# Kernel tuning notes

Hardware: AMD Instinct MI355X
Metric: run time of the kernel (lower is better)

Reference implementation:

```python
import jax, jax.numpy as jnp
import numpy as np

D_MODEL = 1024
NUM_HEADS = 16
D_K = D_MODEL // NUM_HEADS  # 64
THETA = 10000.0
MAX_SEQ_LEN = 2048


def _trunc_normal(key, shape, std):
    # approximate trunc_normal_(mean=0, std, a=-3*std, b=3*std)
    u = jax.random.truncated_normal(key, -3.0, 3.0, shape, dtype=jnp.float32)
    return u * std


def setup_inputs() -> dict:
    key = jax.random.key(0)
    ks = jax.random.split(key, 5)
    x = jax.random.normal(ks[0], (2, 2048, D_MODEL), dtype=jnp.float32)
    token_positions = jnp.arange(2048, dtype=jnp.int64 if jax.config.jax_enable_x64 else jnp.int32)
    sigma = 2.0 / (D_MODEL + D_MODEL)
    Wq = _trunc_normal(ks[1], (D_MODEL, D_MODEL), sigma)
    Wk = _trunc_normal(ks[2], (D_MODEL, D_MODEL), sigma)
    Wv = _trunc_normal(ks[3], (D_MODEL, D_MODEL), sigma)
    Wo = _trunc_normal(ks[4], (D_MODEL, D_MODEL), sigma)
    return {"in_features": x, "Wq": Wq, "Wk": Wk, "Wv": Wv, "Wo": Wo,
            "token_positions": token_positions}


def _rope(x, cos_phi, sin_phi):
    # x: (..., seq, d_k); cos/sin: (seq, d_k//2)
    x_even = x[..., 0::2]
    x_odd = x[..., 1::2]
    y_even = x_even * cos_phi - x_odd * sin_phi
    y_odd = x_even * sin_phi + x_odd * cos_phi
    # interleave back
    y = jnp.stack([y_even, y_odd], axis=-1)
    return y.reshape(x.shape)


def reference(in_features, Wq, Wk, Wv, Wo, token_positions):
    b, s, d = in_features.shape
    h, dk = NUM_HEADS, D_K
    # projections: weight is (d_out, d_in)
    q = jnp.einsum('bsd,ed->bse', in_features, Wq)
    k = jnp.einsum('bsd,ed->bse', in_features, Wk)
    v = jnp.einsum('bsd,ed->bse', in_features, Wv)
    # split heads: (b, h, s, dk)
    q = q.reshape(b, s, h, dk).transpose(0, 2, 1, 3)
    k = k.reshape(b, s, h, dk).transpose(0, 2, 1, 3)
    v = v.reshape(b, s, h, dk).transpose(0, 2, 1, 3)
    # RoPE tables
    inv_freq = 1.0 / (THETA ** (jnp.arange(0, dk, 2, dtype=jnp.float32) / dk))
    phi = token_positions.astype(jnp.float32)[:, None] * inv_freq[None, :]  # (s, dk/2)
    cos_phi, sin_phi = jnp.cos(phi), jnp.sin(phi)
    q = _rope(q, cos_phi, sin_phi)
    k = _rope(k, cos_phi, sin_phi)
    # causal mask
    mask = jnp.tril(jnp.ones((s, s), dtype=bool))
    scores = jnp.einsum('bhqd,bhkd->bhqk', q, k) / jnp.sqrt(jnp.float32(dk))
    scores = jnp.where(mask, scores, -jnp.inf)
    attn = jax.nn.softmax(scores, axis=-1)
    out = jnp.einsum('bhqk,bhkd->bhqd', attn, v)
    out = out.transpose(0, 2, 1, 3).reshape(b, s, d)
    return jnp.einsum('bsd,ed->bse', out, Wo)
```

## Files before the change

kernel.cpp:

```cpp
#include <hip/hip_runtime.h>
#include <hip/hip_bf16.h>
#include <math.h>

#define S_  2048
#define DM_ 1024

typedef unsigned short u16;
typedef __attribute__((ext_vector_type(8))) short short8;
typedef __attribute__((ext_vector_type(4))) float f32x4;

__device__ __forceinline__ u16 f2bf(float f) {
  unsigned u = __float_as_uint(f);
  u += 0x7fffu + ((u >> 16) & 1u);
  return (u16)(u >> 16);
}
__device__ __forceinline__ float bf2f(u16 h) {
  return __uint_as_float((unsigned)h << 16);
}
__device__ __forceinline__ unsigned pack_bf2(float a, float b) {
  union { __hip_bfloat162 h2; unsigned u; } cv;
  cv.h2 = __float22bfloat162_rn(float2{a, b});
  return cv.u;
}
__device__ __forceinline__ void cp16(const void* g, void* l) {
  __builtin_amdgcn_global_load_lds(
      (const __attribute__((address_space(1))) unsigned*)(uintptr_t)g,
      (__attribute__((address_space(3))) unsigned*)(unsigned)(uintptr_t)l, 16, 0, 0);
}

struct CastArgs { const float* src[5]; u16* dst[5]; int n[5]; };

__global__ __launch_bounds__(256) void cast_kernel(CastArgs a) {
  const int z = blockIdx.y;
  const int i = (blockIdx.x * 256 + threadIdx.x) * 8;
  if (i >= a.n[z]) return;
  const float4* s = (const float4*)(a.src[z] + i);
  float4 v0 = s[0], v1 = s[1];
  short8 r;
  r[0] = (short)f2bf(v0.x); r[1] = (short)f2bf(v0.y);
  r[2] = (short)f2bf(v0.z); r[3] = (short)f2bf(v0.w);
  r[4] = (short)f2bf(v1.x); r[5] = (short)f2bf(v1.y);
  r[6] = (short)f2bf(v1.z); r[7] = (short)f2bf(v1.w);
  *(short8*)(a.dst[z] + i) = r;
}

struct GemmArgs { const u16* A; const u16* W[3]; void* out[3]; int modes; };

template<int GXL>
__global__ __launch_bounds__(256, 2) void gemm_mfma(GemmArgs g) {
  constexpr int BM = 128, BN = 64;
  constexpr int ABYTES = BM * 64 * 2;
  constexpr int SLOT = ABYTES + BN * 64 * 2;
  __shared__ __align__(16) char lds[3 * SLOT];

  const int tid = threadIdx.x, lane = tid & 63, w = tid >> 6;
  const int wm = w >> 1, wn = w & 1;
  const int t = lane & 15, u = lane >> 4;
  const int l3 = lane >> 3, l7 = lane & 7;
  const int z = blockIdx.z;

  const int nwg = (int)gridDim.y << GXL;
  const int flat = (int)blockIdx.x + ((int)blockIdx.y << GXL);
  const int swz = (flat & 7) * (nwg >> 3) + (flat >> 3);
  const int m0 = (swz >> GXL) * BM;
  const int n0 = (swz & ((1 << GXL) - 1)) * BN;

  const u16* __restrict__ A = g.A;
  const u16* __restrict__ W = g.W[z];

  const int axor = l7 << 4;
  const int ksw = (l7 ^ l3) * 8;
  const u16* Ab = A + (size_t)(m0 + l3) * 1024 + ksw;
  const u16* Wb = W + (size_t)(n0 + l3) * 1024 + ksw;

  auto stg = [&](char* sb, int kt) {
    #pragma unroll
    for (int r = 0; r < 4; r++)
      cp16(Ab + (size_t)(w * 4 + r) * 8192 + kt * 64, sb + (w * 4 + r) * 1024);
    #pragma unroll
    for (int r = 0; r < 2; r++)
      cp16(Wb + (size_t)(w * 2 + r) * 8192 + kt * 64, sb + ABYTES + (w * 2 + r) * 1024);
  };

  const f32x4 fz = {0.f, 0.f, 0.f, 0.f};
  f32x4 acc[4][2];
  #pragma unroll
  for (int i = 0; i < 4; i++) { acc[i][0] = fz; acc[i][1] = fz; }

  stg(lds, 0);
  stg(lds + SLOT, 1);
  asm volatile("s_waitcnt vmcnt(6)" ::: "memory");
  __builtin_amdgcn_s_barrier();

  int rs_ = 0, ss_ = 2;
  for (int kt = 0; kt < 16; kt++) {
    const char* cs = lds + rs_ * SLOT;
    if (kt + 2 < 16) stg(lds + ss_ * SLOT, kt + 2);

    short8 af[2][4], bfr[2][2];
    #pragma unroll
    for (int ks = 0; ks < 2; ks++) {
      const int co = (ks * 64 + u * 16) ^ axor;
      const char* ap = cs + (wm * 64 + t) * 128 + co;
      const char* bp = cs + ABYTES + (wn * 32 + t) * 128 + co;
      #pragma unroll
      for (int mf = 0; mf < 4; mf++) af[ks][mf] = *(const short8*)(ap + mf * 2048);
      #pragma unroll
      for (int nf = 0; nf < 2; nf++) bfr[ks][nf] = *(const short8*)(bp + nf * 2048);
    }
    asm volatile("s_waitcnt lgkmcnt(0)" ::: "memory");
    __builtin_amdgcn_sched_barrier(0);
    __builtin_amdgcn_s_setprio(1);
    #pragma unroll
    for (int ks = 0; ks < 2; ks++)
      #pragma unroll
      for (int mf = 0; mf < 4; mf++)
        #pragma unroll
        for (int nf = 0; nf < 2; nf++)
          acc[mf][nf] = __builtin_amdgcn_mfma_f32_16x16x32_bf16(af[ks][mf], bfr[ks][nf], acc[mf][nf], 0, 0, 0);
    __builtin_amdgcn_s_setprio(0);

    if (kt + 2 < 16)      { asm volatile("s_waitcnt vmcnt(6)" ::: "memory"); }
    else if (kt + 1 < 16) { asm volatile("s_waitcnt vmcnt(0)" ::: "memory"); }
    __builtin_amdgcn_s_barrier();
    rs_ = (rs_ == 2) ? 0 : rs_ + 1;
    ss_ = (ss_ == 2) ? 0 : ss_ + 1;
  }

  const int mode = (g.modes >> (2 * z)) & 3;
  const int rbase = m0 + wm * 64 + u * 4;
  const int cbase = n0 + wn * 32 + t;
  if (mode == 0) {
    u16* O = (u16*)g.out[z];
    #pragma unroll
    for (int mt = 0; mt < 4; mt++)
      #pragma unroll
      for (int nt = 0; nt < 2; nt++)
        #pragma unroll
        for (int r = 0; r < 4; r++)
          O[(size_t)(rbase + mt * 16 + r) * 1024 + cbase + nt * 16] = f2bf(acc[mt][nt][r]);
  } else if (mode == 1) {
    u16* O = (u16*)g.out[z];
    #pragma unroll
    for (int mt = 0; mt < 4; mt++)
      #pragma unroll
      for (int nt = 0; nt < 2; nt++) {
        int gr = rbase + mt * 16;
        int b = gr >> 11, s0 = gr & (S_ - 1);
        int gc = cbase + nt * 16;
        int h = gc >> 6, d = gc & 63;
        ushort4 v;
        v.x = f2bf(acc[mt][nt][0]); v.y = f2bf(acc[mt][nt][1]);
        v.z = f2bf(acc[mt][nt][2]); v.w = f2bf(acc[mt][nt][3]);
        *(ushort4*)&O[(size_t)((b * 16 + h) * 64 + d) * 2048 + s0] = v;
      }
  } else {
    float* O = (float*)g.out[z];
    #pragma unroll
    for (int mt = 0; mt < 4; mt++)
      #pragma unroll
      for (int nt = 0; nt < 2; nt++)
        #pragma unroll
        for (int r = 0; r < 4; r++)
          O[(size_t)(rbase + mt * 16 + r) * 1024 + cbase + nt * 16] = acc[mt][nt][r];
  }
}

__global__ __launch_bounds__(256) void rope_kernel(u16* qb, u16* kb, const int* __restrict__ tp) {
  const int isq = (blockIdx.y == 0);
  u16* p = isq ? qb : kb;
  const float outscale = isq ? 0.18033688011112042f : 1.0f;
  const int i = (blockIdx.x * 256 + threadIdx.x) * 8;
  const int s = (i >> 10) & (S_ - 1);
  const int d = i & 63;
  const float pos = (float)tp[s];
  short8 v = *(short8*)(p + i);
  #pragma unroll
  for (int j = 0; j < 4; j++) {
    float inv = exp2f(-(float)(d + 2 * j) * 0.20762050593046439f);
    float phi = pos * inv;
    float sn, cs;
    sincosf(phi, &sn, &cs);
    float xe = bf2f((u16)v[2 * j]), xo = bf2f((u16)v[2 * j + 1]);
    v[2 * j]     = (short)f2bf((xe * cs - xo * sn) * outscale);
    v[2 * j + 1] = (short)f2bf((xe * sn + xo * cs) * outscale);
  }
  *(short8*)(p + i) = v;
}

__global__ __launch_bounds__(512, 4) void attn_mfma(const u16* __restrict__ qb, const u16* __restrict__ kb,
                                                    const u16* __restrict__ vt, u16* __restrict__ ab) {
  __shared__ __align__(16) u16 Qs[2][4096];
  __shared__ __align__(16) u16 Ks[2][4096];
  __shared__ __align__(16) u16 Vs[2][4096];

  const int tid = threadIdx.x, lane = tid & 63, w = tid >> 6;
  const int v = w & 3, g = w >> 2;
  const int t = lane & 15, u = lane >> 4;
  const int bh = blockIdx.y, b = bh >> 4, h = bh & 15;
  const int i = blockIdx.x;
  const int qa = 31 - i;
  const int qbt = i;
  const int nk = 32 - i;
  const size_t qkb = (size_t)b * S_ * 1024 + h * 64;
  const size_t vtb = (size_t)bh * 64 * 2048;

  {
    const int qtile = g ? qbt : qa;
    cp16(qb + qkb + (size_t)(qtile * 64 + lane) * 1024 + v * 8,       (char*)Qs[g] + v * 1024);
    cp16(qb + qkb + (size_t)(qtile * 64 + lane) * 1024 + (v + 4) * 8, (char*)Qs[g] + 4096 + v * 1024);
  }
  cp16(kb + qkb + (size_t)lane * 1024 + w * 8, (char*)Ks[0] + w * 1024);
  cp16(vt + vtb + (size_t)lane * 2048 + w * 8, (char*)Vs[0] + w * 1024);
  __syncthreads();

  short8 aqA[2], aqP[2];
  #pragma unroll
  for (int ks = 0; ks < 2; ks++) {
    aqA[ks] = *(const short8*)((const char*)Qs[0] + (ks * 4 + u) * 1024 + (v * 16 + t) * 16);
    short8 bq = *(const short8*)((const char*)Qs[1] + (ks * 4 + u) * 1024 + (v * 16 + t) * 16);
    aqP[ks] = g ? bq : aqA[ks];
  }

  const f32x4 fzero = {0.f, 0.f, 0.f, 0.f};
  f32x4 oPrim[4], oSec[4];
  #pragma unroll
  for (int ct = 0; ct < 4; ct++) { oPrim[ct] = fzero; oSec[ct] = fzero; }
  float rsumP = 0.f, rsumS = 0.f;

  const int qprim = g ? qbt : qa;
  const int qrowP = qprim * 64 + v * 16 + t;
  const int qrowA = qa * 64 + v * 16 + t;

  for (int kt = 0; kt < nk; kt++) {
    const int cur = kt & 1, nxt = cur ^ 1;
    if (kt + 1 < nk) {
      cp16(kb + qkb + (size_t)((kt + 1) * 64 + lane) * 1024 + w * 8, (char*)Ks[nxt] + w * 1024);
      cp16(vt + vtb + (size_t)lane * 2048 + (kt + 1) * 64 + w * 8,   (char*)Vs[nxt] + w * 1024);
    }

    if (kt <= qbt) {
      f32x4 st[4] = {fzero, fzero, fzero, fzero};
      __builtin_amdgcn_s_setprio(1);
      #pragma unroll
      for (int ks = 0; ks < 2; ks++)
        #pragma unroll
        for (int ct = 0; ct < 4; ct++) {
          short8 kf = *(const short8*)((const char*)Ks[cur] + (ks * 4 + u) * 1024 + (ct * 16 + t) * 16);
          st[ct] = __builtin_amdgcn_mfma_f32_16x16x32_bf16(kf, aqP[ks], st[ct], 0, 0, 0);
        }
      __builtin_amdgcn_s_setprio(0);

      unsigned pb2[4][2];
      if (kt == qprim) {
        #pragma unroll
        for (int ct = 0; ct < 4; ct++) {
          float p[4];
          #pragma unroll
          for (int r = 0; r < 4; r++) {
            int key = kt * 64 + ct * 16 + 4 * u + r;
            float pv = exp2f(st[ct][r]);
            p[r] = (key > qrowP) ? 0.f : pv;
          }
          rsumP += (p[0] + p[1]) + (p[2] + p[3]);
          pb2[ct][0] = pack_bf2(p[0], p[1]);
          pb2[ct][1] = pack_bf2(p[2], p[3]);
        }
      } else {
        #pragma unroll
        for (int ct = 0; ct < 4; ct++) {
          float p[4];
          #pragma unroll
          for (int r = 0; r < 4; r++) p[r] = exp2f(st[ct][r]);
          rsumP += (p[0] + p[1]) + (p[2] + p[3]);
          pb2[ct][0] = pack_bf2(p[0], p[1]);
          pb2[ct][1] = pack_bf2(p[2], p[3]);
        }
      }

      #pragma unroll
      for (int ks = 0; ks < 2; ks++) {
        union { short8 s8; int i4[4]; } pf;
        #pragma unroll
        for (int jj = 0; jj < 4; jj++) {
          int src = 32 * (u & 1) + 16 * (jj >> 1) + t;
          int v0 = __shfl((int)pb2[ks * 2][jj & 1], src, 64);
          int v1 = __shfl((int)pb2[ks * 2 + 1][jj & 1], src, 64);
          pf.i4[jj] = (u >> 1) ? v1 : v0;
        }
        __builtin_amdgcn_s_setprio(1);
        #pragma unroll
        for (int ct = 0; ct < 4; ct++) {
          short8 vf = *(const short8*)((const char*)Vs[cur] + (ks * 4 + u) * 1024 + (ct * 16 + t) * 16);
          oPrim[ct] = __builtin_amdgcn_mfma_f32_16x16x32_bf16(vf, pf.s8, oPrim[ct], 0, 0, 0);
        }
        __builtin_amdgcn_s_setprio(0);
      }
    } else {
      f32x4 st2[2] = {fzero, fzero};
      __builtin_amdgcn_s_setprio(1);
      #pragma unroll
      for (int ks = 0; ks < 2; ks++)
        #pragma unroll
        for (int c = 0; c < 2; c++) {
          short8 kf = *(const short8*)((const char*)Ks[cur] + (ks * 4 + u) * 1024 + ((2 * g + c) * 16 + t) * 16);
          st2[c] = __builtin_amdgcn_mfma_f32_16x16x32_bf16(kf, aqA[ks], st2[c], 0, 0, 0);
        }
      __builtin_amdgcn_s_setprio(0);

      unsigned ph[2][2];
      float rs = 0.f;
      if (kt == qa) {
        #pragma unroll
        for (int c = 0; c < 2; c++) {
          float p[4];
          #pragma unroll
          for (int r = 0; r < 4; r++) {
            int key = kt * 64 + (2 * g + c) * 16 + 4 * u + r;
            float pv = exp2f(st2[c][r]);
            p[r] = (key > qrowA) ? 0.f : pv;
          }
          rs += (p[0] + p[1]) + (p[2] + p[3]);
          ph[c][0] = pack_bf2(p[0], p[1]);
          ph[c][1] = pack_bf2(p[2], p[3]);
        }
      } else {
        #pragma unroll
        for (int c = 0; c < 2; c++) {
          float p[4];
          #pragma unroll
          for (int r = 0; r < 4; r++) p[r] = exp2f(st2[c][r]);
          rs += (p[0] + p[1]) + (p[2] + p[3]);
          ph[c][0] = pack_bf2(p[0], p[1]);
          ph[c][1] = pack_bf2(p[2], p[3]);
        }
      }

      union { short8 s8; int i4[4]; } pf;
      #pragma unroll
      for (int jj = 0; jj < 4; jj++) {
        int src = 32 * (u & 1) + 16 * (jj >> 1) + t;
        int v0 = __shfl((int)ph[0][jj & 1], src, 64);
        int v1 = __shfl((int)ph[1][jj & 1], src, 64);
        pf.i4[jj] = (u >> 1) ? v1 : v0;
      }
      if (g) {
        rsumS += rs;
        __builtin_amdgcn_s_setprio(1);
        #pragma unroll
        for (int ct = 0; ct < 4; ct++) {
          short8 vf = *(const short8*)((const char*)Vs[cur] + (4 + u) * 1024 + (ct * 16 + t) * 16);
          oSec[ct] = __builtin_amdgcn_mfma_f32_16x16x32_bf16(vf, pf.s8, oSec[ct], 0, 0, 0);
        }
        __builtin_amdgcn_s_setprio(0);
      } else {
        rsumP += rs;
        __builtin_amdgcn_s_setprio(1);
        #pragma unroll
        for (int ct = 0; ct < 4; ct++) {
          short8 vf = *(const short8*)((const char*)Vs[cur] + u * 1024 + (ct * 16 + t) * 16);
          oPrim[ct] = __builtin_amdgcn_mfma_f32_16x16x32_bf16(vf, pf.s8, oPrim[ct], 0, 0, 0);
        }
        __builtin_amdgcn_s_setprio(0);
      }
    }
    __syncthreads();
  }

  float* dmpO = (float*)Ks;
  float* dmpR = (float*)Vs;
  if (g) {
    #pragma unroll
    for (int ct = 0; ct < 4; ct++)
      *(f32x4*)&dmpO[(size_t)(v * 64 + lane) * 16 + ct * 4] = oSec[ct];
    dmpR[v * 64 + lane] = rsumS;
    float rs = rsumP;
    rs += __shfl_xor(rs, 16, 64);
    rs += __shfl_xor(rs, 32, 64);
    const float inv = 1.0f / rs;
    #pragma unroll
    for (int ct = 0; ct < 4; ct++) {
      ushort4 vv;
      vv.x = f2bf(oPrim[ct][0] * inv); vv.y = f2bf(oPrim[ct][1] * inv);
      vv.z = f2bf(oPrim[ct][2] * inv); vv.w = f2bf(oPrim[ct][3] * inv);
      *(ushort4*)&ab[((size_t)b * S_ + qrowP) * 1024 + h * 64 + ct * 16 + 4 * u] = vv;
    }
  }
  __syncthreads();
  if (!g) {
    #pragma unroll
    for (int ct = 0; ct < 4; ct++) {
      f32x4 add = *(const f32x4*)&dmpO[(size_t)(v * 64 + lane) * 16 + ct * 4];
      oPrim[ct] += add;
    }
    float rs = rsumP + dmpR[v * 64 + lane];
    rs += __shfl_xor(rs, 16, 64);
    rs += __shfl_xor(rs, 32, 64);
    const float inv = 1.0f / rs;
    #pragma unroll
    for (int ct = 0; ct < 4; ct++) {
      ushort4 vv;
      vv.x = f2bf(oPrim[ct][0] * inv); vv.y = f2bf(oPrim[ct][1] * inv);
      vv.z = f2bf(oPrim[ct][2] * inv); vv.w = f2bf(oPrim[ct][3] * inv);
      *(ushort4*)&ab[((size_t)b * S_ + qrowA) * 1024 + h * 64 + ct * 16 + 4 * u] = vv;
    }
  }
}

extern "C" void kernel_launch(void* const* d_in, const int* in_sizes, int n_in,
                              void* d_out, int out_size, void* d_ws, size_t ws_size,
                              hipStream_t stream) {
  const float* x  = (const float*)d_in[0];
  const float* Wq = (const float*)d_in[1];
  const float* Wk = (const float*)d_in[2];
  const float* Wv = (const float*)d_in[3];
  const float* Wo = (const float*)d_in[4];
  const int*   tp = (const int*)d_in[5];
  float* out = (float*)d_out;

  char* ws = (char*)d_ws;
  u16* xb  = (u16*)(ws);
  u16* wqb = (u16*)(ws + (8 << 20));
  u16* wkb = (u16*)(ws + (10 << 20));
  u16* wvb = (u16*)(ws + (12 << 20));
  u16* wob = (u16*)(ws + (14 << 20));
  u16* qbuf = (u16*)(ws + (16 << 20));
  u16* kbuf = (u16*)(ws + (24 << 20));
  u16* vtb  = (u16*)(ws + (32 << 20));
  u16* abuf = (u16*)(ws + (40 << 20));

  CastArgs ca;
  ca.src[0] = x;  ca.dst[0] = xb;  ca.n[0] = 2 * S_ * DM_;
  ca.src[1] = Wq; ca.dst[1] = wqb; ca.n[1] = DM_ * DM_;
  ca.src[2] = Wk; ca.dst[2] = wkb; ca.n[2] = DM_ * DM_;
  ca.src[3] = Wv; ca.dst[3] = wvb; ca.n[3] = DM_ * DM_;
  ca.src[4] = Wo; ca.dst[4] = wob; ca.n[4] = DM_ * DM_;
  cast_kernel<<<dim3(2048, 5), 256, 0, stream>>>(ca);

  GemmArgs gq;
  gq.A = xb;
  gq.W[0] = wqb; gq.W[1] = wkb; gq.W[2] = wvb;
  gq.out[0] = qbuf; gq.out[1] = kbuf; gq.out[2] = vtb;
  gq.modes = (1 << 4);
  gemm_mfma<4><<<dim3(16, 32, 3), 256, 0, stream>>>(gq);

  rope_kernel<<<dim3(2048, 2), 256, 0, stream>>>(qbuf, kbuf, tp);

  attn_mfma<<<dim3(16, 32), 512, 0, stream>>>(qbuf, kbuf, vtb, abuf);

  GemmArgs go;
  go.A = abuf;
  go.W[0] = wob; go.W[1] = wob; go.W[2] = wob;
  go.out[0] = out; go.out[1] = out; go.out[2] = out;
  go.modes = 2;
  gemm_mfma<4><<<dim3(16, 32, 1), 256, 0, stream>>>(go);
}
```

Measured before the change: 183.9 us.

## Double attention query tile to 128 rows per warp group to reuse K/V

Each attention block now processes two 64-row query sub-tiles per pair (128-row tiles), so every K/V tile loaded to LDS feeds twice as many MFMAs, and the grid shrinks from 16 to 8 blocks along the query axis. The causal pairing of a short and a long tile is kept at 128-row granularity. This is meant to cut K/V global and LDS traffic per unit of work. In exchange it doubles accumulator and fragment registers, lowers the occupancy hint from 4 to 2, and launches half as many blocks, which may underfill the device.

```diff
diff --git a/kernel.cpp b/kernel.cpp
--- a/kernel.cpp
+++ b/kernel.cpp
@@ -188,9 +188,9 @@
   *(short8*)(p + i) = v;
 }
 
-__global__ __launch_bounds__(512, 4) void attn_mfma(const u16* __restrict__ qb, const u16* __restrict__ kb,
+__global__ __launch_bounds__(512, 2) void attn_mfma(const u16* __restrict__ qb, const u16* __restrict__ kb,
                                                     const u16* __restrict__ vt, u16* __restrict__ ab) {
-  __shared__ __align__(16) u16 Qs[2][4096];
+  __shared__ __align__(16) u16 Qs[2][8192];
   __shared__ __align__(16) u16 Ks[2][4096];
   __shared__ __align__(16) u16 Vs[2][4096];
 
@@ -199,38 +199,51 @@
   const int t = lane & 15, u = lane >> 4;
   const int bh = blockIdx.y, b = bh >> 4, h = bh & 15;
   const int i = blockIdx.x;
-  const int qa = 31 - i;
+  const int qat = 15 - i;
   const int qbt = i;
-  const int nk = 32 - i;
+  const int nk = 32 - 2 * i;
   const size_t qkb = (size_t)b * S_ * 1024 + h * 64;
   const size_t vtb = (size_t)bh * 64 * 2048;
 
   {
-    const int qtile = g ? qbt : qa;
-    cp16(qb + qkb + (size_t)(qtile * 64 + lane) * 1024 + v * 8,       (char*)Qs[g] + v * 1024);
-    cp16(qb + qkb + (size_t)(qtile * 64 + lane) * 1024 + (v + 4) * 8, (char*)Qs[g] + 4096 + v * 1024);
+    const int qtb = (g ? qbt : qat) * 128;
+    #pragma unroll
+    for (int rh = 0; rh < 2; rh++) {
+      cp16(qb + qkb + (size_t)(qtb + rh * 64 + lane) * 1024 + v * 8,
+           (char*)Qs[g] + v * 2048 + rh * 1024 + lane * 16);
+      cp16(qb + qkb + (size_t)(qtb + rh * 64 + lane) * 1024 + (v + 4) * 8,
+           (char*)Qs[g] + (v + 4) * 2048 + rh * 1024 + lane * 16);
+    }
   }
   cp16(kb + qkb + (size_t)lane * 1024 + w * 8, (char*)Ks[0] + w * 1024);
   cp16(vt + vtb + (size_t)lane * 2048 + w * 8, (char*)Vs[0] + w * 1024);
   __syncthreads();
 
-  short8 aqA[2], aqP[2];
+  short8 aqA[2][2], aqP[2][2];
   #pragma unroll
-  for (int ks = 0; ks < 2; ks++) {
-    aqA[ks] = *(const short8*)((const char*)Qs[0] + (ks * 4 + u) * 1024 + (v * 16 + t) * 16);
-    short8 bq = *(const short8*)((const char*)Qs[1] + (ks * 4 + u) * 1024 + (v * 16 + t) * 16);
-    aqP[ks] = g ? bq : aqA[ks];
-  }
+  for (int qf = 0; qf < 2; qf++)
+    #pragma unroll
+    for (int ks = 0; ks < 2; ks++) {
+      aqA[qf][ks] = *(const short8*)((const char*)Qs[0] + (ks * 4 + u) * 2048 + (qf * 64 + v * 16 + t) * 16);
+      short8 bq   = *(const short8*)((const char*)Qs[1] + (ks * 4 + u) * 2048 + (qf * 64 + v * 16 + t) * 16);
+      aqP[qf][ks] = g ? bq : aqA[qf][ks];
+    }
 
   const f32x4 fzero = {0.f, 0.f, 0.f, 0.f};
-  f32x4 oPrim[4], oSec[4];
+  f32x4 oPrim[2][4], oSec[2][4];
   #pragma unroll
-  for (int ct = 0; ct < 4; ct++) { oPrim[ct] = fzero; oSec[ct] = fzero; }
-  float rsumP = 0.f, rsumS = 0.f;
-
-  const int qprim = g ? qbt : qa;
-  const int qrowP = qprim * 64 + v * 16 + t;
-  const int qrowA = qa * 64 + v * 16 + t;
+  for (int qf = 0; qf < 2; qf++)
+    #pragma unroll
+    for (int ct = 0; ct < 4; ct++) { oPrim[qf][ct] = fzero; oSec[qf][ct] = fzero; }
+  float rsumP[2] = {0.f, 0.f}, rsumS[2] = {0.f, 0.f};
+
+  const int qpT = g ? qbt : qat;
+  int qrowP[2], qrowA[2];
+  #pragma unroll
+  for (int qf = 0; qf < 2; qf++) {
+    qrowP[qf] = qpT * 128 + qf * 64 + v * 16 + t;
+    qrowA[qf] = qat * 128 + qf * 64 + v * 16 + t;
+  }
 
   for (int kt = 0; kt < nk; kt++) {
     const int cur = kt & 1, nxt = cur ^ 1;
@@ -239,127 +252,150 @@
       cp16(vt + vtb + (size_t)lane * 2048 + (kt + 1) * 64 + w * 8,   (char*)Vs[nxt] + w * 1024);
     }
 
-    if (kt <= qbt) {
-      f32x4 st[4] = {fzero, fzero, fzero, fzero};
+    if ((kt >> 1) <= qbt) {
+      f32x4 st[2][4];
+      #pragma unroll
+      for (int qf = 0; qf < 2; qf++)
+        #pragma unroll
+        for (int ct = 0; ct < 4; ct++) st[qf][ct] = fzero;
       __builtin_amdgcn_s_setprio(1);
       #pragma unroll
       for (int ks = 0; ks < 2; ks++)
         #pragma unroll
         for (int ct = 0; ct < 4; ct++) {
           short8 kf = *(const short8*)((const char*)Ks[cur] + (ks * 4 + u) * 1024 + (ct * 16 + t) * 16);
-          st[ct] = __builtin_amdgcn_mfma_f32_16x16x32_bf16(kf, aqP[ks], st[ct], 0, 0, 0);
+          st[0][ct] = __builtin_amdgcn_mfma_f32_16x16x32_bf16(kf, aqP[0][ks], st[0][ct], 0, 0, 0);
+          st[1][ct] = __builtin_amdgcn_mfma_f32_16x16x32_bf16(kf, aqP[1][ks], st[1][ct], 0, 0, 0);
         }
       __builtin_amdgcn_s_setprio(0);
 
-      unsigned pb2[4][2];
-      if (kt == qprim) {
+      unsigned pb2[2][4][2];
+      if ((kt >> 1) == qpT) {
+        #pragma unroll
+        for (int qf = 0; qf < 2; qf++)
+          #pragma unroll
+          for (int ct = 0; ct < 4; ct++) {
+            float p[4];
+            #pragma unroll
+            for (int r = 0; r < 4; r++) {
+              int key = kt * 64 + ct * 16 + 4 * u + r;
+              float pv = exp2f(st[qf][ct][r]);
+              p[r] = (key > qrowP[qf]) ? 0.f : pv;
+            }
+            rsumP[qf] += (p[0] + p[1]) + (p[2] + p[3]);
+            pb2[qf][ct][0] = pack_bf2(p[0], p[1]);
+            pb2[qf][ct][1] = pack_bf2(p[2], p[3]);
+          }
+      } else {
+        #pragma unroll
+        for (int qf = 0; qf < 2; qf++)
+          #pragma unroll
+          for (int ct = 0; ct < 4; ct++) {
+            float p[4];
+            #pragma unroll
+            for (int r = 0; r < 4; r++) p[r] = exp2f(st[qf][ct][r]);
+            rsumP[qf] += (p[0] + p[1]) + (p[2] + p[3]);
+            pb2[qf][ct][0] = pack_bf2(p[0], p[1]);
+            pb2[qf][ct][1] = pack_bf2(p[2], p[3]);
+          }
+      }
+
+      #pragma unroll
+      for (int ks = 0; ks < 2; ks++) {
+        union { short8 s8; int i4[4]; } pf[2];
+        #pragma unroll
+        for (int qf = 0; qf < 2; qf++)
+          #pragma unroll
+          for (int jj = 0; jj < 4; jj++) {
+            int src = 32 * (u & 1) + 16 * (jj >> 1) + t;
+            int v0 = __shfl((int)pb2[qf][ks * 2][jj & 1], src, 64);
+            int v1 = __shfl((int)pb2[qf][ks * 2 + 1][jj & 1], src, 64);
+            pf[qf].i4[jj] = (u >> 1) ? v1 : v0;
+          }
+        __builtin_amdgcn_s_setprio(1);
         #pragma unroll
         for (int ct = 0; ct < 4; ct++) {
-          float p[4];
+          short8 vf = *(const short8*)((const char*)Vs[cur] + (ks * 4 + u) * 1024 + (ct * 16 + t) * 16);
+          oPrim[0][ct] = __builtin_amdgcn_mfma_f32_16x16x32_bf16(vf, pf[0].s8, oPrim[0][ct], 0, 0, 0);
+          oPrim[1][ct] = __builtin_amdgcn_mfma_f32_16x16x32_bf16(vf, pf[1].s8, oPrim[1][ct], 0, 0, 0);
+        }
+        __builtin_amdgcn_s_setprio(0);
+      }
+    } else {
+      f32x4 st2[2][2];
+      #pragma unroll
+      for (int qf = 0; qf < 2; qf++) { st2[qf][0] = fzero; st2[qf][1] = fzero; }
+      __builtin_amdgcn_s_setprio(1);
+      #pragma unroll
+      for (int ks = 0; ks < 2; ks++)
+        #pragma unroll
+        for (int c = 0; c < 2; c++) {
+          short8 kf = *(const short8*)((const char*)Ks[cur] + (ks * 4 + u) * 1024 + ((2 * g + c) * 16 + t) * 16);
+          st2[0][c] = __builtin_amdgcn_mfma_f32_16x16x32_bf16(kf, aqA[0][ks], st2[0][c], 0, 0, 0);
+          st2[1][c] = __builtin_amdgcn_mfma_f32_16x16x32_bf16(kf, aqA[1][ks], st2[1][c], 0, 0, 0);
+        }
+      __builtin_amdgcn_s_setprio(0);
+
+      unsigned ph[2][2][2];
+      float rs[2] = {0.f, 0.f};
+      if ((kt >> 1) == qat) {
+        #pragma unroll
+        for (int qf = 0; qf < 2; qf++)
           #pragma unroll
-          for (int r = 0; r < 4; r++) {
-            int key = kt * 64 + ct * 16 + 4 * u + r;
-            float pv = exp2f(st[ct][r]);
-            p[r] = (key > qrowP) ? 0.f : pv;
+          for (int c = 0; c < 2; c++) {
+            float p[4];
+            #pragma unroll
+            for (int r = 0; r < 4; r++) {
+              int key = kt * 64 + (2 * g + c) * 16 + 4 * u + r;
+              float pv = exp2f(st2[qf][c][r]);
+              p[r] = (key > qrowA[qf]) ? 0.f : pv;
+            }
+            rs[qf] += (p[0] + p[1]) + (p[2] + p[3]);
+            ph[qf][c][0] = pack_bf2(p[0], p[1]);
+            ph[qf][c][1] = pack_bf2(p[2], p[3]);
           }
-          rsumP += (p[0] + p[1]) + (p[2] + p[3]);
-          pb2[ct][0] = pack_bf2(p[0], p[1]);
-          pb2[ct][1] = pack_bf2(p[2], p[3]);
-        }
       } else {
         #pragma unroll
-        for (int ct = 0; ct < 4; ct++) {
-          float p[4];
+        for (int qf = 0; qf < 2; qf++)
           #pragma unroll
-          for (int r = 0; r < 4; r++) p[r] = exp2f(st[ct][r]);
-          rsumP += (p[0] + p[1]) + (p[2] + p[3]);
-          pb2[ct][0] = pack_bf2(p[0], p[1]);
-          pb2[ct][1] = pack_bf2(p[2], p[3]);
-        }
-      }
-
-      #pragma unroll
-      for (int ks = 0; ks < 2; ks++) {
-        union { short8 s8; int i4[4]; } pf;
+          for (int c = 0; c < 2; c++) {
+            float p[4];
+            #pragma unroll
+            for (int r = 0; r < 4; r++) p[r] = exp2f(st2[qf][c][r]);
+            rs[qf] += (p[0] + p[1]) + (p[2] + p[3]);
+            ph[qf][c][0] = pack_bf2(p[0], p[1]);
+            ph[qf][c][1] = pack_bf2(p[2], p[3]);
+          }
+      }
+
+      union { short8 s8; int i4[4]; } pf[2];
+      #pragma unroll
+      for (int qf = 0; qf < 2; qf++)
         #pragma unroll
         for (int jj = 0; jj < 4; jj++) {
           int src = 32 * (u & 1) + 16 * (jj >> 1) + t;
-          int v0 = __shfl((int)pb2[ks * 2][jj & 1], src, 64);
-          int v1 = __shfl((int)pb2[ks * 2 + 1][jj & 1], src, 64);
-          pf.i4[jj] = (u >> 1) ? v1 : v0;
+          int v0 = __shfl((int)ph[qf][0][jj & 1], src, 64);
+          int v1 = __shfl((int)ph[qf][1][jj & 1], src, 64);
+          pf[qf].i4[jj] = (u >> 1) ? v1 : v0;
         }
-        __builtin_amdgcn_s_setprio(1);
-        #pragma unroll
-        for (int ct = 0; ct < 4; ct++) {
-          short8 vf = *(const short8*)((const char*)Vs[cur] + (ks * 4 + u) * 1024 + (ct * 16 + t) * 16);
-          oPrim[ct] = __builtin_amdgcn_mfma_f32_16x16x32_bf16(vf, pf.s8, oPrim[ct], 0, 0, 0);
-        }
-        __builtin_amdgcn_s_setprio(0);
-      }
-    } else {
-      f32x4 st2[2] = {fzero, fzero};
-      __builtin_amdgcn_s_setprio(1);
-      #pragma unroll
-      for (int ks = 0; ks < 2; ks++)
-        #pragma unroll
-        for (int c = 0; c < 2; c++) {
-          short8 kf = *(const short8*)((const char*)Ks[cur] + (ks * 4 + u) * 1024 + ((2 * g + c) * 16 + t) * 16);
-          st2[c] = __builtin_amdgcn_mfma_f32_16x16x32_bf16(kf, aqA[ks], st2[c], 0, 0, 0);
-        }
-      __builtin_amdgcn_s_setprio(0);
-
-      unsigned ph[2][2];
-      float rs = 0.f;
-      if (kt == qa) {
-        #pragma unroll
-        for (int c = 0; c < 2; c++) {
-          float p[4];
-          #pragma unroll
-          for (int r = 0; r < 4; r++) {
-            int key = kt * 64 + (2 * g + c) * 16 + 4 * u + r;
-            float pv = exp2f(st2[c][r]);
-            p[r] = (key > qrowA) ? 0.f : pv;
-          }
-          rs += (p[0] + p[1]) + (p[2] + p[3]);
-          ph[c][0] = pack_bf2(p[0], p[1]);
-          ph[c][1] = pack_bf2(p[2], p[3]);
-        }
-      } else {
-        #pragma unroll
-        for (int c = 0; c < 2; c++) {
-          float p[4];
-          #pragma unroll
-          for (int r = 0; r < 4; r++) p[r] = exp2f(st2[c][r]);
-          rs += (p[0] + p[1]) + (p[2] + p[3]);
-          ph[c][0] = pack_bf2(p[0], p[1]);
-          ph[c][1] = pack_bf2(p[2], p[3]);
-        }
-      }
-
-      union { short8 s8; int i4[4]; } pf;
-      #pragma unroll
-      for (int jj = 0; jj < 4; jj++) {
-        int src = 32 * (u & 1) + 16 * (jj >> 1) + t;
-        int v0 = __shfl((int)ph[0][jj & 1], src, 64);
-        int v1 = __shfl((int)ph[1][jj & 1], src, 64);
-        pf.i4[jj] = (u >> 1) ? v1 : v0;
-      }
       if (g) {
-        rsumS += rs;
+        rsumS[0] += rs[0]; rsumS[1] += rs[1];
         __builtin_amdgcn_s_setprio(1);
         #pragma unroll
         for (int ct = 0; ct < 4; ct++) {
           short8 vf = *(const short8*)((const char*)Vs[cur] + (4 + u) * 1024 + (ct * 16 + t) * 16);
-          oSec[ct] = __builtin_amdgcn_mfma_f32_16x16x32_bf16(vf, pf.s8, oSec[ct], 0, 0, 0);
+          oSec[0][ct] = __builtin_amdgcn_mfma_f32_16x16x32_bf16(vf, pf[0].s8, oSec[0][ct], 0, 0, 0);
+          oSec[1][ct] = __builtin_amdgcn_mfma_f32_16x16x32_bf16(vf, pf[1].s8, oSec[1][ct], 0, 0, 0);
         }
         __builtin_amdgcn_s_setprio(0);
       } else {
-        rsumP += rs;
+        rsumP[0] += rs[0]; rsumP[1] += rs[1];
         __builtin_amdgcn_s_setprio(1);
         #pragma unroll
         for (int ct = 0; ct < 4; ct++) {
           short8 vf = *(const short8*)((const char*)Vs[cur] + u * 1024 + (ct * 16 + t) * 16);
-          oPrim[ct] = __builtin_amdgcn_mfma_f32_16x16x32_bf16(vf, pf.s8, oPrim[ct], 0, 0, 0);
+          oPrim[0][ct] = __builtin_amdgcn_mfma_f32_16x16x32_bf16(vf, pf[0].s8, oPrim[0][ct], 0, 0, 0);
+          oPrim[1][ct] = __builtin_amdgcn_mfma_f32_16x16x32_bf16(vf, pf[1].s8, oPrim[1][ct], 0, 0, 0);
         }
         __builtin_amdgcn_s_setprio(0);
       }
@@ -367,42 +403,52 @@
     __syncthreads();
   }
 
-  float* dmpO = (float*)Ks;
-  float* dmpR = (float*)Vs;
+  float* dmp0 = (float*)Ks;
+  float* dmp1 = (float*)Vs;
+  float* dmpR = (float*)Qs;
   if (g) {
     #pragma unroll
-    for (int ct = 0; ct < 4; ct++)
-      *(f32x4*)&dmpO[(size_t)(v * 64 + lane) * 16 + ct * 4] = oSec[ct];
-    dmpR[v * 64 + lane] = rsumS;
-    float rs = rsumP;
-    rs += __shfl_xor(rs, 16, 64);
-    rs += __shfl_xor(rs, 32, 64);
-    const float inv = 1.0f / rs;
-    #pragma unroll
     for (int ct = 0; ct < 4; ct++) {
-      ushort4 vv;
-      vv.x = f2bf(oPrim[ct][0] * inv); vv.y = f2bf(oPrim[ct][1] * inv);
-      vv.z = f2bf(oPrim[ct][2] * inv); vv.w = f2bf(oPrim[ct][3] * inv);
-      *(ushort4*)&ab[((size_t)b * S_ + qrowP) * 1024 + h * 64 + ct * 16 + 4 * u] = vv;
+      *(f32x4*)&dmp0[(size_t)(v * 64 + lane) * 16 + ct * 4] = oSec[0][ct];
+      *(f32x4*)&dmp1[(size_t)(v * 64 + lane) * 16 + ct * 4] = oSec[1][ct];
+    }
+    dmpR[v * 64 + lane]       = rsumS[0];
+    dmpR[256 + v * 64 + lane] = rsumS[1];
+    #pragma unroll
+    for (int qf = 0; qf < 2; qf++) {
+      float rsv = rsumP[qf];
+      rsv += __shfl_xor(rsv, 16, 64);
+      rsv += __shfl_xor(rsv, 32, 64);
+      const float inv = 1.0f / rsv;
+      #pragma unroll
+      for (int ct = 0; ct < 4; ct++) {
+        ushort4 vv;
+        vv.x = f2bf(oPrim[qf][ct][0] * inv); vv.y = f2bf(oPrim[qf][ct][1] * inv);
+        vv.z = f2bf(oPrim[qf][ct][2] * inv); vv.w = f2bf(oPrim[qf][ct][3] * inv);
+        *(ushort4*)&ab[((size_t)b * S_ + qrowP[qf]) * 1024 + h * 64 + ct * 16 + 4 * u] = vv;
+      }
     }
   }
   __syncthreads();
   if (!g) {
     #pragma unroll
     for (int ct = 0; ct < 4; ct++) {
-      f32x4 add = *(const f32x4*)&dmpO[(size_t)(v * 64 + lane) * 16 + ct * 4];
-      oPrim[ct] += add;
-    }
-    float rs = rsumP + dmpR[v * 64 + lane];
-    rs += __shfl_xor(rs, 16, 64);
-    rs += __shfl_xor(rs, 32, 64);
-    const float inv = 1.0f / rs;
-    #pragma unroll
-    for (int ct = 0; ct < 4; ct++) {
-      ushort4 vv;
-      vv.x = f2bf(oPrim[ct][0] * inv); vv.y = f2bf(oPrim[ct][1] * inv);
-      vv.z = f2bf(oPrim[ct][2] * inv); vv.w = f2bf(oPrim[ct][3] * inv);
-      *(ushort4*)&ab[((size_t)b * S_ + qrowA) * 1024 + h * 64 + ct * 16 + 4 * u] = vv;
+      oPrim[0][ct] += *(const f32x4*)&dmp0[(size_t)(v * 64 + lane) * 16 + ct * 4];
+      oPrim[1][ct] += *(const f32x4*)&dmp1[(size_t)(v * 64 + lane) * 16 + ct * 4];
+    }
+    #pragma unroll
+    for (int qf = 0; qf < 2; qf++) {
+      float rsv = rsumP[qf] + dmpR[qf * 256 + v * 64 + lane];
+      rsv += __shfl_xor(rsv, 16, 64);
+      rsv += __shfl_xor(rsv, 32, 64);
+      const float inv = 1.0f / rsv;
+      #pragma unroll
+      for (int ct = 0; ct < 4; ct++) {
+        ushort4 vv;
+        vv.x = f2bf(oPrim[qf][ct][0] * inv); vv.y = f2bf(oPrim[qf][ct][1] * inv);
+        vv.z = f2bf(oPrim[qf][ct][2] * inv); vv.w = f2bf(oPrim[qf][ct][3] * inv);
+        *(ushort4*)&ab[((size_t)b * S_ + qrowA[qf]) * 1024 + h * 64 + ct * 16 + 4 * u] = vv;
+      }
     }
   }
 }
@@ -446,7 +492,7 @@
 
   rope_kernel<<<dim3(2048, 2), 256, 0, stream>>>(qbuf, kbuf, tp);
 
-  attn_mfma<<<dim3(16, 32), 512, 0, stream>>>(qbuf, kbuf, vtb, abuf);
+  attn_mfma<<<dim3(8, 32), 512, 0, stream>>>(qbuf, kbuf, vtb, abuf);
 
   GemmArgs go;
   go.A = abuf;
```

Measured after the change: 187.7 us. 2.1% more time.
